# Performance work log

Hardware: AMD Instinct MI355X
Metric: run time of the kernel (lower is better)

## Reference

```python
import jax, jax.numpy as jnp
import numpy as np

B, C, H, W = 8, 256, 128, 128
K = 3  # conv kernel size, padding=1 -> SAME


def conv3x3(x, w, b):
    # x: [B,C,H,W], w: [O,I,K,K], b: [O]
    y = jax.lax.conv_general_dilated(
        x, w, window_strides=(1, 1), padding='SAME',
        dimension_numbers=('NCHW', 'OIHW', 'NCHW'))
    return y + b[None, :, None, None]


def setup_inputs() -> dict:
    key = jax.random.key(0)
    ks = jax.random.split(key, 7)
    fan_in = C * K * K
    s = 1.0 / np.sqrt(fan_in)
    x = jax.random.normal(ks[0], (B, C, H, W), dtype=jnp.float32)
    Wq = jax.random.uniform(ks[1], (C, C, K, K), jnp.float32, -s, s)
    bq = jax.random.uniform(ks[2], (C,), jnp.float32, -s, s)
    Wk = jax.random.uniform(ks[3], (C, C, K, K), jnp.float32, -s, s)
    bk = jax.random.uniform(ks[4], (C,), jnp.float32, -s, s)
    Wv = jax.random.uniform(ks[5], (C, C, K, K), jnp.float32, -s, s)
    bv = jax.random.uniform(ks[6], (C,), jnp.float32, -s, s)
    return {'x': x, 'Wq': Wq, 'bq': bq, 'Wk': Wk, 'bk': bk, 'Wv': Wv, 'bv': bv}


def reference(x, Wq, bq, Wk, bk, Wv, bv):
    b_, c_, h_, w_ = x.shape
    residual = x
    q = jax.nn.relu(conv3x3(x, Wq, bq))  # [B,C,H,W]
    k = jax.nn.relu(conv3x3(x, Wk, bk))  # [B,C,H,W]
    v = conv3x3(x, Wv, bv)               # [B,C,H,W]
    # per-(batch,channel) spatial matmul: [H,W] @ [H,W] -> [H,W] (requires H==W)
    attn = jnp.einsum('bcij,bcjk->bcik', q, k)
    # softmax over the flattened H*W positions jointly per (b,c)
    attn = jax.nn.softmax(attn.reshape(b_, c_, h_ * w_), axis=-1).reshape(b_, c_, h_, w_)
    y = jnp.einsum('bcij,bcjk->bcik', attn, v)
    return y + residual
```

## Files before the change

kernel.cpp:

```cpp
#include <hip/hip_runtime.h>

#define BB 8
#define CC 256
#define HH 128
#define WW 128
#define HW (HH*WW)

typedef float f32x4 __attribute__((ext_vector_type(4)));
typedef float f32x16 __attribute__((ext_vector_type(16)));
typedef short s16x8 __attribute__((ext_vector_type(8)));

__device__ inline unsigned short f2bf(float f) {
  union { float f; unsigned int u; } un;
  un.f = f;
  unsigned int u = un.u;
  return (unsigned short)((u + 0x7fffu + ((u >> 16) & 1u)) >> 16);
}

__device__ __forceinline__ void gload_lds16(const void* g, void* l) {
  __builtin_amdgcn_global_load_lds(
      (const __attribute__((address_space(1))) unsigned int*)g,
      (__attribute__((address_space(3))) unsigned int*)l, 16, 0, 0);
}

__global__ __launch_bounds__(256) void k_prepass(const float* __restrict__ x,
                                                 unsigned short* __restrict__ xbf) {
  __shared__ float tile[64][68];
  int bh = blockIdx.x;
  int b = bh >> 7, h = bh & 127;
  int w0 = blockIdx.y * 64;
  int c0 = blockIdx.z * 64;
  int t = threadIdx.x;
  {
    int c = t >> 2, wq = (t & 3) << 4;
    const float4* src = reinterpret_cast<const float4*>(
        x + (((size_t)(b * CC + c0 + c) * HH + h) * WW + w0 + wq));
    float4 v0 = src[0], v1 = src[1], v2 = src[2], v3 = src[3];
    *reinterpret_cast<float4*>(&tile[c][wq + 0])  = v0;
    *reinterpret_cast<float4*>(&tile[c][wq + 4])  = v1;
    *reinterpret_cast<float4*>(&tile[c][wq + 8])  = v2;
    *reinterpret_cast<float4*>(&tile[c][wq + 12]) = v3;
  }
  __syncthreads();
  {
    int w = t >> 2, cg = (t & 3) << 4;
    unsigned short tmp[16];
#pragma unroll
    for (int i = 0; i < 16; ++i) tmp[i] = f2bf(tile[cg + i][w]);
    unsigned short* dst = xbf + ((size_t)(b * HH + h) * WW + w0 + w) * CC + c0 + cg;
    *reinterpret_cast<int4*>(dst)     = *reinterpret_cast<int4*>(tmp);
    *reinterpret_cast<int4*>(dst + 8) = *reinterpret_cast<int4*>(tmp + 8);
  }
}

__global__ __launch_bounds__(256) void k_repack(const float* __restrict__ Wq,
                                                const float* __restrict__ Wk,
                                                const float* __restrict__ Wv,
                                                unsigned short* __restrict__ Wp,
                                                unsigned short* __restrict__ zp) {
  if (blockIdx.x == 0 && threadIdx.x < 64) {
    int4 z = {0, 0, 0, 0};
    reinterpret_cast<int4*>(zp)[threadIdx.x] = z;
  }
  int idx = blockIdx.x * 256 + threadIdx.x;
  if (idx >= 8 * 9 * 768 * 32) return;
  int ci = idx & 31;
  int tmp = idx >> 5;
  int focs = tmp % 768;
  int tmp2 = tmp / 768;
  int tap = tmp2 % 9;
  int chunk = tmp2 / 9;
  int cv = focs >> 8, oc = focs & 255;
  int cin = chunk * 32 + ci;
  const float* Wsrc = (cv == 0) ? Wq : ((cv == 1) ? Wk : Wv);
  Wp[idx] = f2bf(Wsrc[(size_t)(oc * 256 + cin) * 9 + tap]);
}

__global__ __launch_bounds__(256, 2) void k_conv(const unsigned short* __restrict__ xbf,
                                                 const unsigned short* __restrict__ Wp,
                                                 const unsigned short* __restrict__ zp,
                                                 const float* __restrict__ bq,
                                                 const float* __restrict__ bk,
                                                 const float* __restrict__ bv,
                                                 unsigned short* __restrict__ qkv) {
  __shared__ unsigned short xs[2][4][132][32];
  __shared__ float bias_s[128];
  int bid = blockIdx.x;
  int v_ = (bid & 7) * 384 + (bid >> 3);
  int mtile = v_ % 6;
  int bhp = v_ / 6;
  int b = bhp >> 6;
  int h0 = (bhp & 63) * 2;
  int t = threadIdx.x;
  int lane = t & 63, wave = t >> 6;
  int fq = wave;
  int l31 = lane & 31, lg1 = lane >> 5;

  if (t < 128) {
    int focs = mtile * 128 + t;
    int cv = focs >> 8, oc = focs & 255;
    const float* bp = (cv == 0) ? bq : ((cv == 1) ? bk : bv);
    bias_s[t] = bp[oc];
  }
  {
    int cell = t >> 4;
    int bf_ = cell >> 3, r_ = (cell >> 1) & 3;
    int wc_ = (cell & 1) ? 129 : 0;
    *reinterpret_cast<int*>(reinterpret_cast<char*>(&xs[bf_][r_][wc_][0]) + (t & 15) * 4) = 0;
  }

  int l2 = lane >> 2, l4 = lane & 3;
  int osw = l4 ^ (((l2 + 1) >> 1) & 3);
  int hin = h0 + wave - 1;
  bool inb = ((unsigned)hin < 128u);
  const unsigned short* srow =
      xbf + ((size_t)(b * HH + (inb ? hin : 0)) * WW + l2) * CC + osw * 8;
  const unsigned short* zsrc = zp + lane * 8;

  const size_t CH_STRIDE = (size_t)9 * 768 * 32;
  const unsigned short* apbase = Wp + (size_t)(mtile * 128 + fq * 32 + l31) * 32 + lg1 * 8;

  auto STAGE = [&](int bufn, int c) {
    char* d0 = reinterpret_cast<char*>(&xs[bufn][wave][1][0]);
    if (inb) {
      const unsigned short* s0 = srow + c * 32;
#pragma unroll
      for (int j = 0; j < 8; ++j) gload_lds16(s0 + j * (16 * CC), d0 + j * 1024);
    } else {
#pragma unroll
      for (int j = 0; j < 8; ++j) gload_lds16(zsrc, d0 + j * 1024);
    }
  };
  auto ALOAD = [&](s16x8 (&Af)[3], const unsigned short* ap, int un) {
    const int ss = un >> 1, kk = un & 1;
#pragma unroll
    for (int rr = 0; rr < 3; ++rr)
      Af[rr] = *reinterpret_cast<const s16x8*>(ap + (rr * 3 + ss) * (768 * 32) + kk * 16);
  };
  auto BREAD = [&](s16x8 (&Bf)[4], const char* xsb, int un, int nt) {
    const int ss = un >> 1, kk = un & 1;
    const int col = nt * 32 + l31 + ss;
    const int pslot = (kk * 2 + lg1) ^ ((col >> 1) & 3);
#pragma unroll
    for (int rin = 0; rin < 4; ++rin)
      Bf[rin] = *reinterpret_cast<const s16x8*>(
          xsb + rin * (132 * 64) + col * 64 + pslot * 16);
  };

  f32x16 acc[2][4] = {};
  s16x8 Afb[2][3];
  s16x8 Bfb[2][4];

  STAGE(0, 0);
  ALOAD(Afb[0], apbase, 0);
  asm volatile("s_waitcnt vmcnt(3)" ::: "memory");
  __builtin_amdgcn_s_barrier();
  BREAD(Bfb[0], reinterpret_cast<const char*>(&xs[0][0][0][0]), 0, 0);

  for (int chunk = 0; chunk < 8; ++chunk) {
    const int buf = chunk & 1;
    const unsigned short* ap_cur = apbase + chunk * CH_STRIDE;
    const char* xsb = reinterpret_cast<const char*>(&xs[buf][0][0][0]);

#pragma unroll
    for (int u = 0; u < 6; ++u) {
#pragma unroll
      for (int nt = 0; nt < 4; ++nt) {
        if (nt < 3) {
          BREAD(Bfb[(nt + 1) & 1], xsb, u, nt + 1);
        } else if (u < 5) {
          BREAD(Bfb[0], xsb, u + 1, 0);
        }
        if (nt == 0) {
          if (u < 5) ALOAD(Afb[(u + 1) & 1], ap_cur, u + 1);
          else if (chunk < 7) ALOAD(Afb[0], ap_cur + CH_STRIDE, 0);
          if (u < 4 && chunk < 7) {
            char* dstg = reinterpret_cast<char*>(&xs[buf ^ 1][wave][1][0]);
            if (inb) {
              const unsigned short* s0 = srow + (chunk + 1) * 32;
              gload_lds16(s0 + (2 * u) * (16 * CC), dstg + (2 * u) * 1024);
              gload_lds16(s0 + (2 * u + 1) * (16 * CC), dstg + (2 * u + 1) * 1024);
            } else {
              gload_lds16(zsrc, dstg + (2 * u) * 1024);
              gload_lds16(zsrc, dstg + (2 * u + 1) * 1024);
            }
          }
        }
        __builtin_amdgcn_sched_barrier(0);
        __builtin_amdgcn_s_setprio(1);
#pragma unroll
        for (int rr = 0; rr < 3; ++rr)
#pragma unroll
          for (int row = 0; row < 2; ++row)
            acc[row][nt] = __builtin_amdgcn_mfma_f32_32x32x16_bf16(
                Afb[u & 1][rr], Bfb[nt & 1][row + rr], acc[row][nt], 0, 0, 0);
        __builtin_amdgcn_s_setprio(0);
        __builtin_amdgcn_sched_barrier(0);
      }
    }
    if (chunk < 7) {
      asm volatile("s_waitcnt vmcnt(6)" ::: "memory");
      __builtin_amdgcn_s_barrier();
      asm volatile("" ::: "memory");
      BREAD(Bfb[0], reinterpret_cast<const char*>(&xs[buf ^ 1][0][0][0]), 0, 0);
    }
  }

#pragma unroll
  for (int row = 0; row < 2; ++row) {
#pragma unroll
    for (int nt = 0; nt < 4; ++nt) {
      int wcol = nt * 32 + l31;
      int h = h0 + row;
#pragma unroll
      for (int reg = 0; reg < 16; ++reg) {
        int rloc = (reg & 3) + 8 * (reg >> 2) + 4 * lg1;
        int floc = fq * 32 + rloc;
        float vv = acc[row][nt][reg] + bias_s[floc];
        int focs = mtile * 128 + floc;
        if (focs < 512) vv = fmaxf(vv, 0.0f);
        int cv = focs >> 8, oc = focs & 255;
        qkv[(size_t)(cv * 2048 + b * 256 + oc) * HW + h * WW + wcol] = f2bf(vv);
      }
    }
  }
}

#define PADA 136
__global__ __launch_bounds__(256) void k_attn(const unsigned short* __restrict__ qkv,
                                              const float* __restrict__ x,
                                              float* __restrict__ out) {
  __shared__ unsigned short al[128][PADA];
  __shared__ unsigned short kt[128][PADA];
  __shared__ unsigned short vt[128][PADA];
  __shared__ float red[8];
  int bc = blockIdx.x;
  const unsigned short* qp = qkv + (size_t)bc * HW;
  const unsigned short* kp = qkv + (size_t)(2048 + bc) * HW;
  const unsigned short* vp = qkv + (size_t)(4096 + bc) * HW;
  int t = threadIdx.x;
  for (int g = t; g < HW; g += 256) {
    int row = g >> 7, col = g & 127;
    kt[col][row] = kp[g];
    vt[col][row] = vp[g];
  }
  __syncthreads();
  int lane = t & 63, wave = t >> 6;
  int wm = wave >> 1, wn = wave & 1;
  int l15 = lane & 15, lg = lane >> 4;
  f32x4 acc[4][4] = {};
#pragma unroll
  for (int kk = 0; kk < 4; ++kk) {
    s16x8 af[4], bfr[4];
#pragma unroll
    for (int m = 0; m < 4; ++m)
      af[m] = *reinterpret_cast<const s16x8*>(qp + (size_t)(wm * 64 + m * 16 + l15) * WW + kk * 32 + lg * 8);
#pragma unroll
    for (int n = 0; n < 4; ++n)
      bfr[n] = *reinterpret_cast<const s16x8*>(&kt[wn * 64 + n * 16 + l15][kk * 32 + lg * 8]);
#pragma unroll
    for (int m = 0; m < 4; ++m)
#pragma unroll
      for (int n = 0; n < 4; ++n)
        acc[m][n] = __builtin_amdgcn_mfma_f32_16x16x32_bf16(af[m], bfr[n], acc[m][n], 0, 0, 0);
  }
  float lm = -3.0e38f;
#pragma unroll
  for (int m = 0; m < 4; ++m)
#pragma unroll
    for (int n = 0; n < 4; ++n)
#pragma unroll
      for (int rg = 0; rg < 4; ++rg)
        lm = fmaxf(lm, acc[m][n][rg]);
  for (int off = 32; off > 0; off >>= 1) lm = fmaxf(lm, __shfl_xor(lm, off));
  if (lane == 0) red[wave] = lm;
  __syncthreads();
  float M = fmaxf(fmaxf(red[0], red[1]), fmaxf(red[2], red[3]));
  float ls = 0.0f;
#pragma unroll
  for (int m = 0; m < 4; ++m)
#pragma unroll
    for (int n = 0; n < 4; ++n)
#pragma unroll
      for (int rg = 0; rg < 4; ++rg)
        ls += __expf(acc[m][n][rg] - M);
  for (int off = 32; off > 0; off >>= 1) ls += __shfl_xor(ls, off);
  if (lane == 0) red[4 + wave] = ls;
  __syncthreads();
  float inv = 1.0f / (red[4] + red[5] + red[6] + red[7]);
#pragma unroll
  for (int m = 0; m < 4; ++m) {
#pragma unroll
    for (int n = 0; n < 4; ++n) {
      int col = wn * 64 + n * 16 + l15;
#pragma unroll
      for (int rg = 0; rg < 4; ++rg) {
        int row = wm * 64 + m * 16 + lg * 4 + rg;
        al[row][col] = f2bf(__expf(acc[m][n][rg] - M) * inv);
      }
    }
  }
  __syncthreads();
  f32x4 o_[4][4] = {};
#pragma unroll
  for (int kk = 0; kk < 4; ++kk) {
    s16x8 af[4], bfr[4];
#pragma unroll
    for (int m = 0; m < 4; ++m)
      af[m] = *reinterpret_cast<const s16x8*>(&al[wm * 64 + m * 16 + l15][kk * 32 + lg * 8]);
#pragma unroll
    for (int n = 0; n < 4; ++n)
      bfr[n] = *reinterpret_cast<const s16x8*>(&vt[wn * 64 + n * 16 + l15][kk * 32 + lg * 8]);
#pragma unroll
    for (int m = 0; m < 4; ++m)
#pragma unroll
      for (int n = 0; n < 4; ++n)
        o_[m][n] = __builtin_amdgcn_mfma_f32_16x16x32_bf16(af[m], bfr[n], o_[m][n], 0, 0, 0);
  }
  const float* xp = x + (size_t)bc * HW;
  float* op = out + (size_t)bc * HW;
#pragma unroll
  for (int m = 0; m < 4; ++m) {
#pragma unroll
    for (int n = 0; n < 4; ++n) {
      int col = wn * 64 + n * 16 + l15;
#pragma unroll
      for (int rg = 0; rg < 4; ++rg) {
        int row = wm * 64 + m * 16 + lg * 4 + rg;
        op[row * WW + col] = o_[m][n][rg] + xp[row * WW + col];
      }
    }
  }
}

extern "C" void kernel_launch(void* const* d_in, const int* in_sizes, int n_in,
                              void* d_out, int out_size, void* d_ws, size_t ws_size,
                              hipStream_t stream) {
  const float* x  = (const float*)d_in[0];
  const float* Wq = (const float*)d_in[1];
  const float* bq = (const float*)d_in[2];
  const float* Wk = (const float*)d_in[3];
  const float* bk = (const float*)d_in[4];
  const float* Wv = (const float*)d_in[5];
  const float* bv = (const float*)d_in[6];
  float* out = (float*)d_out;

  unsigned short* xbf = (unsigned short*)d_ws;
  unsigned short* qkv = xbf + (size_t)33554432;
  unsigned short* Wp  = qkv + (size_t)3 * 33554432;
  unsigned short* zp  = Wp + (size_t)(8 * 9 * 768 * 32);

  dim3 g0(1024, 2, 4);
  k_prepass<<<g0, 256, 0, stream>>>(x, xbf);
  k_repack<<<6912, 256, 0, stream>>>(Wq, Wk, Wv, Wp, zp);
  k_conv<<<3072, 256, 0, stream>>>(xbf, Wp, zp, bq, bk, bv, qkv);
  k_attn<<<2048, 256, 0, stream>>>(qkv, x, out);
}
```

Baseline: 557.9 us.

## Split conv block into 2x2 wave grid and reorder block-to-tile mapping

Each conv block's four waves now form a 2x2 grid over output channels and width: each wave computes 64 filters over 64 columns instead of 32 filters over all 128 columns. This halves the per-wave LDS B-fragment reads per MFMA, at the cost of doubling the per-wave weight (A) register loads and raising the vmcnt wait thresholds. The block index mapping is also changed so consecutive blocks share a weight tile (mtile-major), which changes cache reuse of weights versus input rows.

Measured after the change: 580.0 us. 4.0% more time.

```diff
diff --git a/kernel.cpp b/kernel.cpp
--- a/kernel.cpp
+++ b/kernel.cpp
@@ -87,13 +87,13 @@
   __shared__ float bias_s[128];
   int bid = blockIdx.x;
   int v_ = (bid & 7) * 384 + (bid >> 3);
-  int mtile = v_ % 6;
-  int bhp = v_ / 6;
+  int mtile = v_ / 512;
+  int bhp = v_ % 512;
   int b = bhp >> 6;
   int h0 = (bhp & 63) * 2;
   int t = threadIdx.x;
   int lane = t & 63, wave = t >> 6;
-  int fq = wave;
+  int fh = wave >> 1, cs = wave & 1;
   int l31 = lane & 31, lg1 = lane >> 5;
 
   if (t < 128) {
@@ -118,28 +118,31 @@
   const unsigned short* zsrc = zp + lane * 8;
 
   const size_t CH_STRIDE = (size_t)9 * 768 * 32;
-  const unsigned short* apbase = Wp + (size_t)(mtile * 128 + fq * 32 + l31) * 32 + lg1 * 8;
-
-  auto STAGE = [&](int bufn, int c) {
+  const unsigned short* apbase = Wp + (size_t)(mtile * 128 + fh * 64 + l31) * 32 + lg1 * 8;
+
+  auto STAGE2 = [&](int bufn, int c, int u) {
     char* d0 = reinterpret_cast<char*>(&xs[bufn][wave][1][0]);
     if (inb) {
       const unsigned short* s0 = srow + c * 32;
-#pragma unroll
-      for (int j = 0; j < 8; ++j) gload_lds16(s0 + j * (16 * CC), d0 + j * 1024);
+      gload_lds16(s0 + (2 * u) * (16 * CC), d0 + (2 * u) * 1024);
+      gload_lds16(s0 + (2 * u + 1) * (16 * CC), d0 + (2 * u + 1) * 1024);
     } else {
-#pragma unroll
-      for (int j = 0; j < 8; ++j) gload_lds16(zsrc, d0 + j * 1024);
+      gload_lds16(zsrc, d0 + (2 * u) * 1024);
+      gload_lds16(zsrc, d0 + (2 * u + 1) * 1024);
     }
   };
-  auto ALOAD = [&](s16x8 (&Af)[3], const unsigned short* ap, int un) {
+  auto ALOAD = [&](s16x8 (&Af)[3][2], const unsigned short* ap, int un) {
     const int ss = un >> 1, kk = un & 1;
 #pragma unroll
     for (int rr = 0; rr < 3; ++rr)
-      Af[rr] = *reinterpret_cast<const s16x8*>(ap + (rr * 3 + ss) * (768 * 32) + kk * 16);
+#pragma unroll
+      for (int mt = 0; mt < 2; ++mt)
+        Af[rr][mt] = *reinterpret_cast<const s16x8*>(
+            ap + (rr * 3 + ss) * (768 * 32) + mt * 1024 + kk * 16);
   };
   auto BREAD = [&](s16x8 (&Bf)[4], const char* xsb, int un, int nt) {
     const int ss = un >> 1, kk = un & 1;
-    const int col = nt * 32 + l31 + ss;
+    const int col = cs * 64 + nt * 32 + l31 + ss;
     const int pslot = (kk * 2 + lg1) ^ ((col >> 1) & 3);
 #pragma unroll
     for (int rin = 0; rin < 4; ++rin)
@@ -147,13 +150,22 @@
           xsb + rin * (132 * 64) + col * 64 + pslot * 16);
   };
 
-  f32x16 acc[2][4] = {};
-  s16x8 Afb[2][3];
+  f32x16 acc[2][2][2] = {};
+  s16x8 Afb[2][3][2];
   s16x8 Bfb[2][4];
 
-  STAGE(0, 0);
+  {
+    char* d0 = reinterpret_cast<char*>(&xs[0][wave][1][0]);
+    if (inb) {
+#pragma unroll
+      for (int j = 0; j < 8; ++j) gload_lds16(srow + j * (16 * CC), d0 + j * 1024);
+    } else {
+#pragma unroll
+      for (int j = 0; j < 8; ++j) gload_lds16(zsrc, d0 + j * 1024);
+    }
+  }
   ALOAD(Afb[0], apbase, 0);
-  asm volatile("s_waitcnt vmcnt(3)" ::: "memory");
+  asm volatile("s_waitcnt vmcnt(6)" ::: "memory");
   __builtin_amdgcn_s_barrier();
   BREAD(Bfb[0], reinterpret_cast<const char*>(&xs[0][0][0][0]), 0, 0);
 
@@ -165,41 +177,31 @@
 #pragma unroll
     for (int u = 0; u < 6; ++u) {
 #pragma unroll
-      for (int nt = 0; nt < 4; ++nt) {
-        if (nt < 3) {
-          BREAD(Bfb[(nt + 1) & 1], xsb, u, nt + 1);
+      for (int sc = 0; sc < 2; ++sc) {
+        if (sc == 0) {
+          if (u < 5) ALOAD(Afb[(u + 1) & 1], ap_cur, u + 1);
+          else if (chunk < 7) ALOAD(Afb[0], ap_cur + CH_STRIDE, 0);
+          if (u < 4 && chunk < 7) STAGE2(buf ^ 1, chunk + 1, u);
+          BREAD(Bfb[1], xsb, u, 1);
         } else if (u < 5) {
           BREAD(Bfb[0], xsb, u + 1, 0);
         }
-        if (nt == 0) {
-          if (u < 5) ALOAD(Afb[(u + 1) & 1], ap_cur, u + 1);
-          else if (chunk < 7) ALOAD(Afb[0], ap_cur + CH_STRIDE, 0);
-          if (u < 4 && chunk < 7) {
-            char* dstg = reinterpret_cast<char*>(&xs[buf ^ 1][wave][1][0]);
-            if (inb) {
-              const unsigned short* s0 = srow + (chunk + 1) * 32;
-              gload_lds16(s0 + (2 * u) * (16 * CC), dstg + (2 * u) * 1024);
-              gload_lds16(s0 + (2 * u + 1) * (16 * CC), dstg + (2 * u + 1) * 1024);
-            } else {
-              gload_lds16(zsrc, dstg + (2 * u) * 1024);
-              gload_lds16(zsrc, dstg + (2 * u + 1) * 1024);
-            }
-          }
-        }
         __builtin_amdgcn_sched_barrier(0);
         __builtin_amdgcn_s_setprio(1);
 #pragma unroll
         for (int rr = 0; rr < 3; ++rr)
 #pragma unroll
           for (int row = 0; row < 2; ++row)
-            acc[row][nt] = __builtin_amdgcn_mfma_f32_32x32x16_bf16(
-                Afb[u & 1][rr], Bfb[nt & 1][row + rr], acc[row][nt], 0, 0, 0);
+#pragma unroll
+            for (int mt = 0; mt < 2; ++mt)
+              acc[mt][row][sc] = __builtin_amdgcn_mfma_f32_32x32x16_bf16(
+                  Afb[u & 1][rr][mt], Bfb[sc & 1][row + rr], acc[mt][row][sc], 0, 0, 0);
         __builtin_amdgcn_s_setprio(0);
         __builtin_amdgcn_sched_barrier(0);
       }
     }
     if (chunk < 7) {
-      asm volatile("s_waitcnt vmcnt(6)" ::: "memory");
+      asm volatile("s_waitcnt vmcnt(12)" ::: "memory");
       __builtin_amdgcn_s_barrier();
       asm volatile("" ::: "memory");
       BREAD(Bfb[0], reinterpret_cast<const char*>(&xs[buf ^ 1][0][0][0]), 0, 0);
@@ -207,20 +209,23 @@
   }
 
 #pragma unroll
-  for (int row = 0; row < 2; ++row) {
-#pragma unroll
-    for (int nt = 0; nt < 4; ++nt) {
-      int wcol = nt * 32 + l31;
-      int h = h0 + row;
-#pragma unroll
-      for (int reg = 0; reg < 16; ++reg) {
-        int rloc = (reg & 3) + 8 * (reg >> 2) + 4 * lg1;
-        int floc = fq * 32 + rloc;
-        float vv = acc[row][nt][reg] + bias_s[floc];
-        int focs = mtile * 128 + floc;
-        if (focs < 512) vv = fmaxf(vv, 0.0f);
-        int cv = focs >> 8, oc = focs & 255;
-        qkv[(size_t)(cv * 2048 + b * 256 + oc) * HW + h * WW + wcol] = f2bf(vv);
+  for (int mt = 0; mt < 2; ++mt) {
+#pragma unroll
+    for (int row = 0; row < 2; ++row) {
+#pragma unroll
+      for (int nt = 0; nt < 2; ++nt) {
+        int wcol = cs * 64 + nt * 32 + l31;
+        int h = h0 + row;
+#pragma unroll
+        for (int reg = 0; reg < 16; ++reg) {
+          int rloc = (reg & 3) + 8 * (reg >> 2) + 4 * lg1;
+          int floc = fh * 64 + mt * 32 + rloc;
+          float vv = acc[mt][row][nt][reg] + bias_s[floc];
+          int focs = mtile * 128 + floc;
+          if (focs < 512) vv = fmaxf(vv, 0.0f);
+          int cv = focs >> 8, oc = focs & 255;
+          qkv[(size_t)(cv * 2048 + b * 256 + oc) * HW + h * WW + wcol] = f2bf(vv);
+        }
       }
     }
   }
```

## Split conv tiles into half-width columns for higher occupancy; alias attn LDS buffer

Applied to the files above, without the earlier changes.

The conv kernel now covers 64 output columns per block instead of 128, which doubles the grid, halves the LDS staging buffer and halves the accumulator registers. Launch bounds rise to 3 blocks per CU. Halo columns are loaded explicitly per stage, with per-lane pointers that fall back to a zero source at image edges, and the MFMA loop is restructured for two column tiles. Separately, the attention kernel reuses the K-transpose LDS buffer for the attention matrix to cut LDS use. The trade-off is more redundant halo and weight loads per output, and the buffer aliasing risks a hazard if K is still being read when the attention matrix is written.

Result: slower. 579.5 us (+3.9%).

```diff
diff --git a/kernel.cpp b/kernel.cpp
--- a/kernel.cpp
+++ b/kernel.cpp
@@ -76,25 +76,29 @@
   Wp[idx] = f2bf(Wsrc[(size_t)(oc * 256 + cin) * 9 + tap]);
 }
 
-__global__ __launch_bounds__(256, 2) void k_conv(const unsigned short* __restrict__ xbf,
+__global__ __launch_bounds__(256, 3) void k_conv(const unsigned short* __restrict__ xbf,
                                                  const unsigned short* __restrict__ Wp,
                                                  const unsigned short* __restrict__ zp,
                                                  const float* __restrict__ bq,
                                                  const float* __restrict__ bk,
                                                  const float* __restrict__ bv,
                                                  unsigned short* __restrict__ qkv) {
-  __shared__ unsigned short xs[2][4][132][32];
+  __shared__ unsigned short xs[2][4][66][32];
   __shared__ float bias_s[128];
   int bid = blockIdx.x;
-  int v_ = (bid & 7) * 384 + (bid >> 3);
+  int v_ = (bid & 7) * 768 + (bid >> 3);
   int mtile = v_ % 6;
-  int bhp = v_ / 6;
+  int r2 = v_ / 6;
+  int whalf = r2 & 1;
+  int bhp = r2 >> 1;
   int b = bhp >> 6;
   int h0 = (bhp & 63) * 2;
+  int w0 = whalf * 64;
   int t = threadIdx.x;
   int lane = t & 63, wave = t >> 6;
   int fq = wave;
   int l31 = lane & 31, lg1 = lane >> 5;
+  int l2 = lane >> 2, l4 = lane & 3;
 
   if (t < 128) {
     int focs = mtile * 128 + t;
@@ -102,40 +106,44 @@
     const float* bp = (cv == 0) ? bq : ((cv == 1) ? bk : bv);
     bias_s[t] = bp[oc];
   }
-  {
-    int cell = t >> 4;
-    int bf_ = cell >> 3, r_ = (cell >> 1) & 3;
-    int wc_ = (cell & 1) ? 129 : 0;
-    *reinterpret_cast<int*>(reinterpret_cast<char*>(&xs[bf_][r_][wc_][0]) + (t & 15) * 4) = 0;
-  }
-
-  int l2 = lane >> 2, l4 = lane & 3;
-  int osw = l4 ^ (((l2 + 1) >> 1) & 3);
+
   int hin = h0 + wave - 1;
-  bool inb = ((unsigned)hin < 128u);
-  const unsigned short* srow =
-      xbf + ((size_t)(b * HH + (inb ? hin : 0)) * WW + l2) * CC + osw * 8;
+  bool hok = ((unsigned)hin < 128u);
+  const unsigned short* rowbase =
+      xbf + (size_t)(b * HH + (hok ? hin : 0)) * WW * CC;
   const unsigned short* zsrc = zp + lane * 8;
+  const int Sarr[5] = {0, 16, 32, 48, 50};
+  const unsigned short* srcp[5];
+  int step[5];
+#pragma unroll
+  for (int i = 0; i < 5; ++i) {
+    int S = Sarr[i];
+    int osw = l4 ^ (((S + l2) >> 1) & 3);
+    int gw = w0 - 1 + S + l2;
+    bool valid = hok && ((unsigned)gw < 128u);
+    srcp[i] = valid ? (rowbase + (size_t)gw * CC + osw * 8) : zsrc;
+    step[i] = valid ? 64 : 0;
+  }
 
   const size_t CH_STRIDE = (size_t)9 * 768 * 32;
   const unsigned short* apbase = Wp + (size_t)(mtile * 128 + fq * 32 + l31) * 32 + lg1 * 8;
 
-  auto STAGE = [&](int bufn, int c) {
-    char* d0 = reinterpret_cast<char*>(&xs[bufn][wave][1][0]);
-    if (inb) {
-      const unsigned short* s0 = srow + c * 32;
-#pragma unroll
-      for (int j = 0; j < 8; ++j) gload_lds16(s0 + j * (16 * CC), d0 + j * 1024);
-    } else {
-#pragma unroll
-      for (int j = 0; j < 8; ++j) gload_lds16(zsrc, d0 + j * 1024);
-    }
+  f32x16 acc[2][2] = {};
+  s16x8 Afb[2][3];
+  s16x8 Bfb[2][4];
+
+  auto STAGEOP = [&](int bufn, int i, int S) {
+    char* dst = reinterpret_cast<char*>(&xs[bufn][wave][0][0]) + S * 64;
+    gload_lds16(srcp[i], dst);
+    srcp[i] = reinterpret_cast<const unsigned short*>(
+        reinterpret_cast<const char*>(srcp[i]) + step[i]);
   };
   auto ALOAD = [&](s16x8 (&Af)[3], const unsigned short* ap, int un) {
     const int ss = un >> 1, kk = un & 1;
 #pragma unroll
     for (int rr = 0; rr < 3; ++rr)
-      Af[rr] = *reinterpret_cast<const s16x8*>(ap + (rr * 3 + ss) * (768 * 32) + kk * 16);
+      Af[rr] = *reinterpret_cast<const s16x8*>(
+          ap + (rr * 3 + ss) * (768 * 32) + kk * 16);
   };
   auto BREAD = [&](s16x8 (&Bf)[4], const char* xsb, int un, int nt) {
     const int ss = un >> 1, kk = un & 1;
@@ -144,14 +152,11 @@
 #pragma unroll
     for (int rin = 0; rin < 4; ++rin)
       Bf[rin] = *reinterpret_cast<const s16x8*>(
-          xsb + rin * (132 * 64) + col * 64 + pslot * 16);
+          xsb + rin * (66 * 64) + col * 64 + pslot * 16);
   };
 
-  f32x16 acc[2][4] = {};
-  s16x8 Afb[2][3];
-  s16x8 Bfb[2][4];
-
-  STAGE(0, 0);
+#pragma unroll
+  for (int i = 0; i < 5; ++i) STAGEOP(0, i, Sarr[i]);
   ALOAD(Afb[0], apbase, 0);
   asm volatile("s_waitcnt vmcnt(3)" ::: "memory");
   __builtin_amdgcn_s_barrier();
@@ -164,42 +169,34 @@
 
 #pragma unroll
     for (int u = 0; u < 6; ++u) {
-#pragma unroll
-      for (int nt = 0; nt < 4; ++nt) {
-        if (nt < 3) {
-          BREAD(Bfb[(nt + 1) & 1], xsb, u, nt + 1);
-        } else if (u < 5) {
-          BREAD(Bfb[0], xsb, u + 1, 0);
-        }
-        if (nt == 0) {
-          if (u < 5) ALOAD(Afb[(u + 1) & 1], ap_cur, u + 1);
-          else if (chunk < 7) ALOAD(Afb[0], ap_cur + CH_STRIDE, 0);
-          if (u < 4 && chunk < 7) {
-            char* dstg = reinterpret_cast<char*>(&xs[buf ^ 1][wave][1][0]);
-            if (inb) {
-              const unsigned short* s0 = srow + (chunk + 1) * 32;
-              gload_lds16(s0 + (2 * u) * (16 * CC), dstg + (2 * u) * 1024);
-              gload_lds16(s0 + (2 * u + 1) * (16 * CC), dstg + (2 * u + 1) * 1024);
-            } else {
-              gload_lds16(zsrc, dstg + (2 * u) * 1024);
-              gload_lds16(zsrc, dstg + (2 * u + 1) * 1024);
-            }
-          }
-        }
-        __builtin_amdgcn_sched_barrier(0);
-        __builtin_amdgcn_s_setprio(1);
-#pragma unroll
-        for (int rr = 0; rr < 3; ++rr)
-#pragma unroll
-          for (int row = 0; row < 2; ++row)
-            acc[row][nt] = __builtin_amdgcn_mfma_f32_32x32x16_bf16(
-                Afb[u & 1][rr], Bfb[nt & 1][row + rr], acc[row][nt], 0, 0, 0);
-        __builtin_amdgcn_s_setprio(0);
-        __builtin_amdgcn_sched_barrier(0);
-      }
+      if (u < 5) ALOAD(Afb[(u + 1) & 1], ap_cur, u + 1);
+      else if (chunk < 7) ALOAD(Afb[0], ap_cur + CH_STRIDE, 0);
+      if (u < 5 && chunk < 7) STAGEOP(buf ^ 1, u, Sarr[u]);
+      BREAD(Bfb[1], xsb, u, 1);
+      __builtin_amdgcn_sched_barrier(0);
+      __builtin_amdgcn_s_setprio(1);
+#pragma unroll
+      for (int rr = 0; rr < 3; ++rr)
+#pragma unroll
+        for (int row = 0; row < 2; ++row)
+          acc[row][0] = __builtin_amdgcn_mfma_f32_32x32x16_bf16(
+              Afb[u & 1][rr], Bfb[0][row + rr], acc[row][0], 0, 0, 0);
+      __builtin_amdgcn_s_setprio(0);
+      __builtin_amdgcn_sched_barrier(0);
+      if (u < 5) BREAD(Bfb[0], xsb, u + 1, 0);
+      __builtin_amdgcn_sched_barrier(0);
+      __builtin_amdgcn_s_setprio(1);
+#pragma unroll
+      for (int rr = 0; rr < 3; ++rr)
+#pragma unroll
+        for (int row = 0; row < 2; ++row)
+          acc[row][1] = __builtin_amdgcn_mfma_f32_32x32x16_bf16(
+              Afb[u & 1][rr], Bfb[1][row + rr], acc[row][1], 0, 0, 0);
+      __builtin_amdgcn_s_setprio(0);
+      __builtin_amdgcn_sched_barrier(0);
     }
     if (chunk < 7) {
-      asm volatile("s_waitcnt vmcnt(6)" ::: "memory");
+      asm volatile("s_waitcnt vmcnt(3)" ::: "memory");
       __builtin_amdgcn_s_barrier();
       asm volatile("" ::: "memory");
       BREAD(Bfb[0], reinterpret_cast<const char*>(&xs[buf ^ 1][0][0][0]), 0, 0);
@@ -209,8 +206,8 @@
 #pragma unroll
   for (int row = 0; row < 2; ++row) {
 #pragma unroll
-    for (int nt = 0; nt < 4; ++nt) {
-      int wcol = nt * 32 + l31;
+    for (int nt = 0; nt < 2; ++nt) {
+      int wcol = w0 + nt * 32 + l31;
       int h = h0 + row;
 #pragma unroll
       for (int reg = 0; reg < 16; ++reg) {
@@ -230,10 +227,10 @@
 __global__ __launch_bounds__(256) void k_attn(const unsigned short* __restrict__ qkv,
                                               const float* __restrict__ x,
                                               float* __restrict__ out) {
-  __shared__ unsigned short al[128][PADA];
   __shared__ unsigned short kt[128][PADA];
   __shared__ unsigned short vt[128][PADA];
   __shared__ float red[8];
+  unsigned short (*al)[PADA] = kt;
   int bc = blockIdx.x;
   const unsigned short* qp = qkv + (size_t)bc * HW;
   const unsigned short* kp = qkv + (size_t)(2048 + bc) * HW;
@@ -353,6 +350,6 @@
   dim3 g0(1024, 2, 4);
   k_prepass<<<g0, 256, 0, stream>>>(x, xbf);
   k_repack<<<6912, 256, 0, stream>>>(Wq, Wk, Wv, Wp, zp);
-  k_conv<<<3072, 256, 0, stream>>>(xbf, Wp, zp, bq, bk, bv, qkv);
+  k_conv<<<6144, 256, 0, stream>>>(xbf, Wp, zp, bq, bk, bv, qkv);
   k_attn<<<2048, 256, 0, stream>>>(qkv, x, out);
 }
```
